# Kernel optimization log

Hardware: AMD Instinct MI355X
Metric: run time of the kernel (lower is better)

## Reference

```python
import jax, jax.numpy as jnp
import numpy as np

HIDDEN = 256
PA = 32          # pairwise_attention_size
PW = 64          # pairwise_size
B, L = 4, 512


def setup_inputs() -> dict:
    key = jax.random.key(0)
    k1, k2, k3, k4, k5, k6 = jax.random.split(key, 6)
    s_in = 1.0 / np.sqrt(HIDDEN)
    s_out = 1.0 / np.sqrt(PA * PA)
    return {
        "hidden_states": jax.random.normal(k1, (B, L, HIDDEN), dtype=jnp.float32),
        "pairwise_states": jax.random.normal(k2, (B, L, L, PW), dtype=jnp.float32),
        "W_in": jax.random.uniform(k3, (PA, HIDDEN), jnp.float32, -s_in, s_in),
        "b_in": jax.random.uniform(k4, (PA,), jnp.float32, -s_in, s_in),
        "W_out": jax.random.uniform(k5, (PW, PA * PA), jnp.float32, -s_out, s_out),
        "b_out": jax.random.uniform(k6, (PW,), jnp.float32, -s_out, s_out),
    }


def reference(hidden_states, pairwise_states, W_in, b_in, W_out, b_out):
    # in_proj: [B, L, H] -> [B, L, PA]
    h = jnp.einsum("blh,ph->blp", hidden_states, W_in) + b_in
    # Original math: triangle[b,i,j,p,q] = h[b,j,p] * h[b,i,q], flattened (p major)
    # then out_proj. Algebraically reorder to avoid the [B,L,L,PA^2] intermediate:
    # out[b,i,j,o] = sum_{p,q} W_out[o, p*PA+q] * h[b,j,p] * h[b,i,q] + b_out[o]
    Wr = W_out.reshape(W_out.shape[0], PA, PA)  # [O, p, q]
    t = jnp.einsum("bjp,opq->bjoq", h, Wr)       # small: [B, L, O, PA]
    out = jnp.einsum("bjoq,biq->bijo", t, h) + b_out
    return out + pairwise_states
```

## Files before the change

### kernel.cpp

```cpp
#include <hip/hip_runtime.h>

#define BB  4
#define LL  512
#define HID 256
#define PAi 32
#define OO  64

using bf16x8 = __attribute__((ext_vector_type(8))) short;
using f32x4  = __attribute__((ext_vector_type(4))) float;

__device__ inline ushort f2bf(float x) {
    union { float f; unsigned u; } v; v.f = x;
    unsigned r = (v.u + 0x7fff + ((v.u >> 16) & 1)) >> 16;
    return (ushort)r;
}

__global__ __launch_bounds__(256) void k_in(const float* __restrict__ hidden,
                                            const float* __restrict__ W_in,
                                            const float* __restrict__ b_in,
                                            float* __restrict__ h,
                                            ushort* __restrict__ hb) {
    __shared__ float4 hid[8 * 64];
    const int tid  = threadIdx.x;
    const int row0 = blockIdx.x * 8;
    const float4* src = (const float4*)(hidden + (size_t)row0 * HID);
    hid[tid]       = src[tid];
    hid[tid + 256] = src[tid + 256];
    __syncthreads();
    const int p = tid & 31;
    const int r = tid >> 5;
    const float4* w = (const float4*)(W_in + (size_t)p * HID);
    float acc = 0.f;
#pragma unroll
    for (int k = 0; k < 64; ++k) {
        float4 hv = hid[r * 64 + k];
        float4 wv = w[k];
        acc += hv.x * wv.x + hv.y * wv.y + hv.z * wv.z + hv.w * wv.w;
    }
    const float val = acc + b_in[p];
    h[(size_t)(row0 + r) * PAi + p]  = val;
    hb[(size_t)(row0 + r) * PAi + p] = f2bf(val);
}

#define RMID 16
__global__ __launch_bounds__(256) void k_mid(const float* __restrict__ h,
                                             const float* __restrict__ W_out,
                                             ushort* __restrict__ t) {
    __shared__ __attribute__((aligned(16))) float hst[PAi][RMID];
    const int tid  = threadIdx.x;
    const int row0 = blockIdx.x * RMID;
    for (int s = tid; s < RMID * PAi; s += 256) {
        const int r = s >> 5, p = s & 31;
        hst[p][r] = h[(size_t)(row0 + r) * PAi + p];
    }
    __syncthreads();
    const int qg = tid & 7;
    const int o1 = tid >> 3;
    const float4* W4 = (const float4*)W_out;
    float4 accA[RMID], accB[RMID];
#pragma unroll
    for (int r = 0; r < RMID; ++r) {
        accA[r] = float4{0, 0, 0, 0};
        accB[r] = float4{0, 0, 0, 0};
    }
#pragma unroll 2
    for (int p = 0; p < PAi; ++p) {
        const float4 wa = W4[(o1 * PAi + p) * 8 + qg];
        const float4 wb = W4[((o1 + 32) * PAi + p) * 8 + qg];
#pragma unroll
        for (int r4 = 0; r4 < RMID / 4; ++r4) {
            const float4 h4 = *(const float4*)&hst[p][r4 * 4];
            const float hr[4] = {h4.x, h4.y, h4.z, h4.w};
#pragma unroll
            for (int e = 0; e < 4; ++e) {
                const int r = r4 * 4 + e;
                accA[r].x += hr[e] * wa.x; accA[r].y += hr[e] * wa.y;
                accA[r].z += hr[e] * wa.z; accA[r].w += hr[e] * wa.w;
                accB[r].x += hr[e] * wb.x; accB[r].y += hr[e] * wb.y;
                accB[r].z += hr[e] * wb.z; accB[r].w += hr[e] * wb.w;
            }
        }
    }
#pragma unroll
    for (int r = 0; r < RMID; ++r) {
        ushort4 ua, ub;
        ua.x = f2bf(accA[r].x); ua.y = f2bf(accA[r].y); ua.z = f2bf(accA[r].z); ua.w = f2bf(accA[r].w);
        ub.x = f2bf(accB[r].x); ub.y = f2bf(accB[r].y); ub.z = f2bf(accB[r].z); ub.w = f2bf(accB[r].w);
        ushort* dst = t + (size_t)(row0 + r) * OO * PAi;
        *(ushort4*)(dst + (o1 * 8 + qg) * 4)        = ua;
        *(ushort4*)(dst + ((o1 + 32) * 8 + qg) * 4) = ub;
    }
}

#define SEG 4096
#define CH  256
#define NCH (SEG / CH)
#define LSTR 260
__global__ __launch_bounds__(256, 4) void k_out(const ushort* __restrict__ t,
                                                const ushort* __restrict__ hb,
                                                const float* __restrict__ pw,
                                                const float* __restrict__ b_out,
                                                float* __restrict__ out) {
    __shared__ float sacc0[16 * LSTR];
    __shared__ float sacc1[16 * LSTR];
    const int tid  = threadIdx.x;
    const int lane = tid & 63;
    const int wave = tid >> 6;
    const int b    = blockIdx.z;
    const int i0   = blockIdx.y * 16;
    const int seg0 = blockIdx.x * SEG;
    const int l15  = lane & 15;
    const int g    = lane >> 4;

    const bf16x8 hfrag = *(const bf16x8*)(hb + ((size_t)(b * LL + i0 + l15)) * PAi + g * 8);
    const f32x4 bo4 = *(const f32x4*)(b_out + ((lane * 4) & 63));
    const size_t outrow0 = ((size_t)(b * LL + i0)) * (LL * OO);

    auto loadA = [&](int c, bf16x8* tf, f32x4* pv) {
        const int cbase = seg0 + c * CH;
#pragma unroll
        for (int rr = 0; rr < 4; ++rr)
            pv[rr] = *(const f32x4*)(pw + outrow0 + (size_t)(wave * 4 + rr) * (LL * OO) + cbase + lane * 4);
        const ushort* tb0 = t + ((size_t)b * LL * OO + cbase + wave * 64 + l15) * PAi + g * 8;
#pragma unroll
        for (int tt = 0; tt < 4; ++tt)
            tf[tt] = *(const bf16x8*)(tb0 + (size_t)tt * (16 * PAi));
    };
    auto mfmaB = [&](const bf16x8* tf, float* sbuf) {
#pragma unroll
        for (int tt = 0; tt < 4; ++tt) {
            f32x4 z = {0.f, 0.f, 0.f, 0.f};
            f32x4 a = __builtin_amdgcn_mfma_f32_16x16x32_bf16(tf[tt], hfrag, z, 0, 0, 0);
            *(f32x4*)&sbuf[l15 * LSTR + wave * 64 + tt * 16 + g * 4] = a;
        }
    };
    auto consC = [&](int c, const f32x4* pv, const float* sbuf) {
        const int cbase = seg0 + c * CH;
#pragma unroll
        for (int rr = 0; rr < 4; ++rr) {
            const int row = wave * 4 + rr;
            const f32x4 a4 = *(const f32x4*)&sbuf[row * LSTR + lane * 4];
            f32x4 res = a4 + bo4 + pv[rr];
            __builtin_nontemporal_store(res,
                (f32x4*)(out + outrow0 + (size_t)row * (LL * OO) + cbase + lane * 4));
        }
    };

    bf16x8 tf0[4], tf1[4];
    f32x4  pv0[4], pv1[4];

    loadA(0, tf0, pv0);
    loadA(1, tf1, pv1);
    mfmaB(tf0, sacc0);
    __syncthreads();

    for (int c = 0; c < NCH; c += 2) {
        consC(c, pv0, sacc0);
        if (c + 2 < NCH) loadA(c + 2, tf0, pv0);
        if (c + 1 < NCH) mfmaB(tf1, sacc1);
        __syncthreads();
        if (c + 1 >= NCH) break;
        consC(c + 1, pv1, sacc1);
        if (c + 3 < NCH) loadA(c + 3, tf1, pv1);
        if (c + 2 < NCH) mfmaB(tf0, sacc0);
        __syncthreads();
    }
}

extern "C" void kernel_launch(void* const* d_in, const int* in_sizes, int n_in,
                              void* d_out, int out_size, void* d_ws, size_t ws_size,
                              hipStream_t stream) {
    const float* hidden = (const float*)d_in[0];
    const float* pw     = (const float*)d_in[1];
    const float* W_in   = (const float*)d_in[2];
    const float* b_in   = (const float*)d_in[3];
    const float* W_out  = (const float*)d_in[4];
    const float* b_out  = (const float*)d_in[5];
    float* out = (float*)d_out;

    float*  h  = (float*)d_ws;
    ushort* hb = (ushort*)(h + (size_t)BB * LL * PAi);
    ushort* tb = hb + (size_t)BB * LL * PAi;

    k_in <<<dim3(BB * LL / 8), 256, 0, stream>>>(hidden, W_in, b_in, h, hb);
    k_mid<<<dim3(BB * LL / RMID), 256, 0, stream>>>(h, W_out, tb);
    k_out<<<dim3(LL * OO / SEG, LL / 16, BB), 256, 0, stream>>>(tb, hb, pw, b_out, out);
}
```

Before: 133.9 us.

## Reuse t fragments across four i-tiles in k_out with deeper pw prefetch

k_out now handles 64 i-rows per block instead of 16, with a 1024-column segment instead of 4096. Each loaded t fragment is reused across four h fragments, which cuts redundant t reads from global memory. The pairwise-state loads are now triple-buffered two steps ahead, and there is one barrier per 16-row step. The kernel stays bound by the large pw read and out write, so gains depend on overlap, and the extra barriers and registers may hurt occupancy.

```diff
diff --git a/kernel.cpp b/kernel.cpp
--- a/kernel.cpp
+++ b/kernel.cpp
@@ -92,78 +92,87 @@
     }
 }
 
-#define SEG 4096
-#define CH  256
-#define NCH (SEG / CH)
+#define SEG  1024
+#define CH   256
+#define NCH  (SEG / CH)
 #define LSTR 260
 __global__ __launch_bounds__(256, 4) void k_out(const ushort* __restrict__ t,
                                                 const ushort* __restrict__ hb,
                                                 const float* __restrict__ pw,
                                                 const float* __restrict__ b_out,
                                                 float* __restrict__ out) {
-    __shared__ float sacc0[16 * LSTR];
-    __shared__ float sacc1[16 * LSTR];
+    __shared__ float s0[16 * LSTR];
+    __shared__ float s1[16 * LSTR];
     const int tid  = threadIdx.x;
     const int lane = tid & 63;
     const int wave = tid >> 6;
     const int b    = blockIdx.z;
-    const int i0   = blockIdx.y * 16;
+    const int i0   = blockIdx.y * 64;
     const int seg0 = blockIdx.x * SEG;
     const int l15  = lane & 15;
     const int g    = lane >> 4;
 
-    const bf16x8 hfrag = *(const bf16x8*)(hb + ((size_t)(b * LL + i0 + l15)) * PAi + g * 8);
+    bf16x8 hf[4];
+#pragma unroll
+    for (int it = 0; it < 4; ++it)
+        hf[it] = *(const bf16x8*)(hb + ((size_t)(b * LL + i0 + it * 16 + l15)) * PAi + g * 8);
+
     const f32x4 bo4 = *(const f32x4*)(b_out + ((lane * 4) & 63));
     const size_t outrow0 = ((size_t)(b * LL + i0)) * (LL * OO);
 
-    auto loadA = [&](int c, bf16x8* tf, f32x4* pv) {
-        const int cbase = seg0 + c * CH;
-#pragma unroll
-        for (int rr = 0; rr < 4; ++rr)
-            pv[rr] = *(const f32x4*)(pw + outrow0 + (size_t)(wave * 4 + rr) * (LL * OO) + cbase + lane * 4);
-        const ushort* tb0 = t + ((size_t)b * LL * OO + cbase + wave * 64 + l15) * PAi + g * 8;
+    auto loadT = [&](int c, bf16x8* tf) {
+        const ushort* tb0 = t + ((size_t)b * LL * OO + seg0 + c * CH + wave * 64 + l15) * PAi + g * 8;
 #pragma unroll
         for (int tt = 0; tt < 4; ++tt)
             tf[tt] = *(const bf16x8*)(tb0 + (size_t)tt * (16 * PAi));
     };
-    auto mfmaB = [&](const bf16x8* tf, float* sbuf) {
+    auto loadP = [&](int c, int it, f32x4* pv) {
+        const int cbase = seg0 + c * CH;
+#pragma unroll
+        for (int rr = 0; rr < 4; ++rr)
+            pv[rr] = *(const f32x4*)(pw + outrow0 +
+                         (size_t)(it * 16 + wave * 4 + rr) * (LL * OO) + cbase + lane * 4);
+    };
+    auto mfmaS = [&](const bf16x8* tf, const bf16x8 hfi, float* sbuf) {
 #pragma unroll
         for (int tt = 0; tt < 4; ++tt) {
             f32x4 z = {0.f, 0.f, 0.f, 0.f};
-            f32x4 a = __builtin_amdgcn_mfma_f32_16x16x32_bf16(tf[tt], hfrag, z, 0, 0, 0);
+            f32x4 a = __builtin_amdgcn_mfma_f32_16x16x32_bf16(tf[tt], hfi, z, 0, 0, 0);
             *(f32x4*)&sbuf[l15 * LSTR + wave * 64 + tt * 16 + g * 4] = a;
         }
     };
-    auto consC = [&](int c, const f32x4* pv, const float* sbuf) {
+    auto consume = [&](int c, int it, const f32x4* pv, const float* sbuf) {
         const int cbase = seg0 + c * CH;
 #pragma unroll
         for (int rr = 0; rr < 4; ++rr) {
-            const int row = wave * 4 + rr;
-            const f32x4 a4 = *(const f32x4*)&sbuf[row * LSTR + lane * 4];
+            const f32x4 a4 = *(const f32x4*)&sbuf[(wave * 4 + rr) * LSTR + lane * 4];
             f32x4 res = a4 + bo4 + pv[rr];
-            __builtin_nontemporal_store(res,
-                (f32x4*)(out + outrow0 + (size_t)row * (LL * OO) + cbase + lane * 4));
+            __builtin_nontemporal_store(res, (f32x4*)(out + outrow0 +
+                (size_t)(it * 16 + wave * 4 + rr) * (LL * OO) + cbase + lane * 4));
         }
     };
 
-    bf16x8 tf0[4], tf1[4];
-    f32x4  pv0[4], pv1[4];
+    bf16x8 tfA[4], tfB[4];
+    f32x4  pv[3][4];
 
-    loadA(0, tf0, pv0);
-    loadA(1, tf1, pv1);
-    mfmaB(tf0, sacc0);
-    __syncthreads();
+    loadT(0, tfA);
+    loadP(0, 0, pv[0]);
+    loadP(0, 1, pv[1]);
 
-    for (int c = 0; c < NCH; c += 2) {
-        consC(c, pv0, sacc0);
-        if (c + 2 < NCH) loadA(c + 2, tf0, pv0);
-        if (c + 1 < NCH) mfmaB(tf1, sacc1);
-        __syncthreads();
-        if (c + 1 >= NCH) break;
-        consC(c + 1, pv1, sacc1);
-        if (c + 3 < NCH) loadA(c + 3, tf1, pv1);
-        if (c + 2 < NCH) mfmaB(tf0, sacc0);
-        __syncthreads();
+#pragma unroll
+    for (int c = 0; c < NCH; ++c) {
+#pragma unroll
+        for (int it = 0; it < 4; ++it) {
+            const int s = c * 4 + it;
+            if (s + 2 < NCH * 4) {
+                const int ns = s + 2;
+                loadP(ns >> 2, ns & 3, pv[ns % 3]);
+            }
+            if (it == 0 && c + 1 < NCH) loadT(c + 1, (c & 1) ? tfA : tfB);
+            mfmaS((c & 1) ? tfB : tfA, hf[it], (s & 1) ? s1 : s0);
+            __syncthreads();
+            consume(c, it, pv[s % 3], (s & 1) ? s1 : s0);
+        }
     }
 }
 
@@ -184,5 +193,5 @@
 
     k_in <<<dim3(BB * LL / 8), 256, 0, stream>>>(hidden, W_in, b_in, h, hb);
     k_mid<<<dim3(BB * LL / RMID), 256, 0, stream>>>(h, W_out, tb);
-    k_out<<<dim3(LL * OO / SEG, LL / 16, BB), 256, 0, stream>>>(tb, hb, pw, b_out, out);
+    k_out<<<dim3(LL * OO / SEG, LL / 64, BB), 256, 0, stream>>>(tb, hb, pw, b_out, out);
 }
```

Result: slower. 188.9 us (+41.1%).
